# Kernel tuning notes

Hardware: AMD Instinct MI355X
Metric: run time of the kernel (lower is better)

Reference implementation:

```python
import jax, jax.numpy as jnp
import numpy as np

B, LQ, LD = 64, 20, 512
D, NB, WIN = 300, 11, 5
EQ, ED, DESC, KC = 5, 10, 20, 10
VW, VE, VC = 50000, 10000, 5000

# KNRM kernel centers / widths (requires_grad=False buffers in the original)
MU = jnp.array([1.0, 0.9, 0.7, 0.5, 0.3, 0.1, -0.1, -0.3, -0.5, -0.7, -0.9], jnp.float32)
SIGMA = jnp.array([1e-3] + [0.1] * 10, jnp.float32)


def setup_inputs() -> dict:
    key = jax.random.key(0)
    ks = jax.random.split(key, 20)
    f = lambda k, s, sc: jax.random.normal(k, s, jnp.float32) * sc
    return {
        "inputs_qwt": jax.random.randint(ks[0], (B, LQ), 0, VW),
        "inputs_qwm": jnp.ones((B, LQ), jnp.float32),
        "inputs_qei": jax.random.randint(ks[1], (B, EQ), 0, VE),
        "inputs_qet": jax.random.randint(ks[2], (B, EQ * DESC), 0, VW),
        "inputs_qew": jax.random.randint(ks[3], (B, EQ * KC), 0, VC),
        "inputs_qem": jnp.ones((B, EQ), jnp.float32),
        "inputs_dwt": jax.random.randint(ks[4], (B, LD), 0, VW),
        "inputs_dwm": jnp.ones((B, LD), jnp.float32),
        "inputs_dei": jax.random.randint(ks[5], (B, ED), 0, VE),
        "inputs_det": jax.random.randint(ks[6], (B, ED * DESC), 0, VW),
        "inputs_dew": jax.random.randint(ks[7], (B, ED * KC), 0, VC),
        "inputs_dem": jnp.ones((B, ED), jnp.float32),
        "wrd_emb": f(ks[8], (VW, D), 0.1),
        "ent_emb": f(ks[9], (VE, 128), 0.1),
        "car_emb": f(ks[10], (VC, 128), 0.1),
        "bow_W": f(ks[11], (128, D), 0.05), "bow_b": jnp.zeros((128,), jnp.float32),
        "conv_uni_W": f(ks[12], (128, 1, D), 0.05), "conv_uni_b": jnp.zeros((128,), jnp.float32),
        "conv_bi_W": f(ks[13], (128, 2, D), 0.04), "conv_bi_b": jnp.zeros((128,), jnp.float32),
        "conv_tri_W": f(ks[14], (128, 3, D), 0.03), "conv_tri_b": jnp.zeros((128,), jnp.float32),
        "conv_des_W": f(ks[15], (128, WIN, D), 0.02), "conv_des_b": jnp.zeros((128,), jnp.float32),
        "dense_f_W": f(ks[16], (1, 16 * NB), 0.1), "dense_f_b": jnp.zeros((1,), jnp.float32),
    }


def _conv_words(x, w, b):
    # x: [N, L, D]; w: [O, k, D] -> relu conv over the word axis, valid padding -> [N, L-k+1, O]
    k, L = w.shape[1], x.shape[1]
    segs = jnp.stack([x[:, i:L - k + 1 + i] for i in range(k)], axis=2)  # [N, L-k+1, k, D]
    return jax.nn.relu(jnp.einsum('nlkd,okd->nlo', segs, w) + b)


def _l2(x):
    return x / jnp.maximum(jnp.linalg.norm(x, axis=-1, keepdims=True), 1e-10)


def _kernel_pool(q, d, mq, md):
    # q:[B,Lq,128] d:[B,Ld,128] mq:[B,Lq] md:[B,Ld] -> [B, NB]
    sim = jnp.einsum('bqe,bde->bqd', q, d)
    pv = jnp.exp(-0.5 * (sim[..., None] - MU) ** 2 / (SIGMA ** 2)) * md[:, None, :, None]
    lps = jnp.log(jnp.maximum(pv.sum(2), 1e-10)) * 0.01 * mq[:, :, None]
    return lps.sum(1)


def _forward(inputs_qwt, inputs_qwm, inputs_qei, inputs_qet, inputs_qew, inputs_qem,
             inputs_dwt, inputs_dwm, inputs_dei, inputs_det, inputs_dew, inputs_dem,
             wrd_emb, ent_emb, car_emb, bow_W, bow_b,
             conv_uni_W, conv_uni_b, conv_bi_W, conv_bi_b, conv_tri_W, conv_tri_b,
             conv_des_W, conv_des_b, dense_f_W, dense_f_b):
    b = inputs_qwt.shape[0]
    qw = wrd_emb[inputs_qwt]  # [B, LQ, D]
    dw = wrd_emb[inputs_dwt]  # [B, LD, D]

    def ent_branch(ids_e, ids_desc, ids_car, n_ent, w_bow):
        desc = wrd_emb[ids_desc].reshape(b * n_ent, DESC, D)
        e_conv = _conv_words(desc, conv_des_W, conv_des_b).max(1).reshape(b, n_ent, 128)
        t = car_emb[ids_car].reshape(b, n_ent * KC, 128)
        att = jax.nn.softmax((w_bow * t).sum(2).reshape(b, n_ent, KC, 1), axis=2)
        ew = (att * t.reshape(b, n_ent, KC, 128)).sum(2)
        return ent_emb[ids_e] + e_conv + ew

    qw_bow = (jnp.einsum('bld,od->blo', qw, bow_W) + bow_b).sum(1, keepdims=True)  # [B,1,128]
    dw_bow = (jnp.einsum('bld,od->blo', dw, bow_W) + bow_b).sum(1, keepdims=True)
    qs = _l2(ent_branch(inputs_qei, inputs_qet, inputs_qew, EQ, qw_bow))  # [B,5,128]
    ds = _l2(ent_branch(inputs_dei, inputs_det, inputs_dew, ED, dw_bow))  # [B,10,128]

    qu = _l2(_conv_words(qw, conv_uni_W, conv_uni_b))
    qb = _l2(_conv_words(qw, conv_bi_W, conv_bi_b))
    qt = _l2(_conv_words(qw, conv_tri_W, conv_tri_b))
    du = _l2(_conv_words(dw, conv_uni_W, conv_uni_b))
    db = _l2(_conv_words(dw, conv_bi_W, conv_bi_b))
    dt = _l2(_conv_words(dw, conv_tri_W, conv_tri_b))

    mqu, mqb, mqt = inputs_qwm, inputs_qwm[:, :-1], inputs_qwm[:, :-2]
    mdu, mdb, mdt = inputs_dwm, inputs_dwm[:, :-1], inputs_dwm[:, :-2]

    kp = _kernel_pool
    pools = [kp(qu, du, mqu, mdu), kp(qu, dt, mqu, mdt), kp(qu, db, mqu, mdb),
             kp(qb, du, mqb, mdu), kp(qt, du, mqt, mdu), kp(qb, db, mqb, mdb),
             kp(qb, dt, mqb, mdt), kp(qt, db, mqt, mdb), kp(qt, dt, mqt, mdt),
             kp(qs, du, inputs_qem, mdu), kp(qs, db, inputs_qem, mdb), kp(qs, dt, inputs_qem, mdt),
             kp(qu, ds, mqu, inputs_dem), kp(qb, ds, mqb, inputs_dem), kp(qt, ds, mqt, inputs_dem),
             kp(qs, ds, inputs_qem, inputs_dem)]
    feats = jnp.concatenate(pools, axis=1)  # [B, 16*NB]
    return jnp.tanh(feats @ dense_f_W.T + dense_f_b)[:, 0]


def reference(inputs_qwt, inputs_qwm, inputs_qei, inputs_qet, inputs_qew, inputs_qem,
              inputs_dwt, inputs_dwm, inputs_dei, inputs_det, inputs_dew, inputs_dem,
              wrd_emb, ent_emb, car_emb, bow_W, bow_b,
              conv_uni_W, conv_uni_b, conv_bi_W, conv_bi_b, conv_tri_W, conv_tri_b,
              conv_des_W, conv_des_b, dense_f_W, dense_f_b):
    return _forward(inputs_qwt, inputs_qwm, inputs_qei, inputs_qet, inputs_qew, inputs_qem,
                    inputs_dwt, inputs_dwm, inputs_dei, inputs_det, inputs_dew, inputs_dem,
                    wrd_emb, ent_emb, car_emb, bow_W, bow_b,
                    conv_uni_W, conv_uni_b, conv_bi_W, conv_bi_b, conv_tri_W, conv_tri_b,
                    conv_des_W, conv_des_b, dense_f_W, dense_f_b)
```

## Files before the change

### kernel.cpp

```cpp
#include <hip/hip_runtime.h>

typedef unsigned short u16;
typedef unsigned int u32;
typedef __attribute__((ext_vector_type(8))) short bf16x8;
typedef __attribute__((ext_vector_type(4))) float f32x4;

#define DEVI __device__ __forceinline__

namespace {
constexpr int LQ_ = 20, LD_ = 512, D_ = 300;
constexpr int EQ_ = 5, ED_ = 10, KC_ = 10;
constexpr int QROWS = 62, DROWS = 1543;
constexpr int QSTR = 64, DSTR = 1600;
constexpr int XDOC0 = 0;
constexpr int XQ0   = 32768;
constexpr int XQD0  = 34048;
constexpr int XDD0  = 40448;
constexpr int XNR   = 53248;
constexpr float MU_H[11] = {1.0f,0.9f,0.7f,0.5f,0.3f,0.1f,-0.1f,-0.3f,-0.5f,-0.7f,-0.9f};
}

__constant__ int P2QT_C[16] = {0,0,0,1,2,1,1,2,2,3,3,3,0,1,2,3};
__constant__ int P2DT_C[16] = {0,2,1,0,0,1,2,1,2,0,1,2,3,3,3,3};
__constant__ int NP_C[4]   = {2,2,4,4};
__constant__ int PPL_C[16] = {0,1,0,0, 2,3,0,0, 2,3,4,5, 4,5,6,7};
__constant__ int SETL_C[16]= {0,0,0,0, 0,0,0,0, 1,1,0,0, 1,1,0,0};

DEVI u16 f2bf(float f){ union{float f;u32 u;} v; v.f=f; u32 r=(v.u+0x7fffu+((v.u>>16)&1u))>>16; return (u16)r; }
DEVI float bf2f(u16 h){ union{u32 u;float f;} v; v.u=((u32)h)<<16; return v.f; }

__global__ __launch_bounds__(256) void k_prep(const int* __restrict__ dwt, const int* __restrict__ qwt,
                                              const int* __restrict__ qet, const int* __restrict__ det,
                                              const float* __restrict__ emb, u16* __restrict__ xall,
                                              const float* __restrict__ Wu, const float* __restrict__ Wb,
                                              const float* __restrict__ Wt, const float* __restrict__ Wd,
                                              u16* __restrict__ Wp){
  const int bx = blockIdx.x;
  if(bx < 16640){
    long idx = (long)bx*256 + threadIdx.x;
    int row = (int)(idx/80), q = (int)(idx - (long)row*80);
    int tid;
    if(row < XQ0) tid = dwt[row];
    else if(row < XQD0) tid = qwt[row-XQ0];
    else if(row < XDD0) tid = qet[row-XQD0];
    else tid = det[row-XDD0];
    ushort4 o4;
    if(q < 75){
      float4 v = ((const float4*)(emb + (long)tid*D_))[q];
      o4.x=f2bf(v.x); o4.y=f2bf(v.y); o4.z=f2bf(v.z); o4.w=f2bf(v.w);
    } else { o4.x=0;o4.y=0;o4.z=0;o4.w=0; }
    *(ushort4*)(xall + (long)row*320 + q*4) = o4;
  } else {
    const int b2 = bx - 16640;
    const int ts = b2/10, ks = b2 - ts*10;
    const float* W; int kk, tap;
    if(ts==0){W=Wu;kk=1;tap=0;}
    else if(ts<3){W=Wb;kk=2;tap=ts-1;}
    else if(ts<6){W=Wt;kk=3;tap=ts-3;}
    else {W=Wd;kk=5;tap=ts-6;}
    for(int idx=threadIdx.x; idx<4096; idx+=256){
      int n0=idx>>9, lane=(idx>>3)&63, j=idx&7;
      int col=lane&15, kg=lane>>4;
      int d=ks*32+kg*8+j, o=n0*16+col;
      float v = (d<300)? W[((long)o*kk + tap)*300 + d] : 0.f;
      Wp[(((long)(ts*8+n0)*10+ks)*64 + lane)*8 + j] = f2bf(v);
    }
  }
}

__global__ __launch_bounds__(512) void k_main(const u16* __restrict__ xall, const u16* __restrict__ Wp,
    const float* __restrict__ bu, const float* __restrict__ bb, const float* __restrict__ bt,
    u16* __restrict__ dcat, u16* __restrict__ qcat, float* __restrict__ parts)
{
  __shared__ __align__(16) char smem[76576];
  const int bx = blockIdx.x, t = threadIdx.x;
  if(bx < 576){
    const bool isdoc = bx < 512;
    const int seq   = isdoc? (bx>>3) : (bx-512);
    const int l0    = isdoc? (bx&7)*64 : 0;
    const int Ltok  = isdoc? LD_ : LQ_;
    const int rowbase = isdoc? XDOC0 : XQ0;
    u16* outp = isdoc? dcat : qcat;
    const long seqstride = isdoc? (long)DSTR*128 : (long)QSTR*128;
    u16* xs = (u16*)smem;
    float* ot = (float*)(smem + 43296);
    const int nrows = min(66, Ltok - l0);
    const u16* src = xall + ((long)(rowbase + seq*Ltok + l0))*320;
    {
      const bf16x8 z = {0,0,0,0,0,0,0,0};
      for(int idx=t; idx<66*40; idx+=512){
        int r=idx/40, cc=idx-r*40;
        bf16x8 v = *(const bf16x8*)&src[(long)r*320 + cc*8];
        *(bf16x8*)&xs[r*328 + cc*8] = (r<nrows)? v : z;
      }
    }
    __syncthreads();
    const int lane=t&63, wave=t>>6;
    const int col16=lane&15, kg=lane>>4;
    #pragma unroll
    for(int c=0;c<3;c++){
      const int tb = (c==0)?0:((c==1)?1:3);
      const int base = (c==0)?0:((c==1)?Ltok:2*Ltok-1);
      const float* bias = (c==0)?bu:((c==1)?bb:bt);
      f32x4 acc4[4];
      #pragma unroll
      for(int mt=0;mt<4;mt++) acc4[mt]=(f32x4){0.f,0.f,0.f,0.f};
      #pragma unroll
      for(int h=0;h<2;h++){
        bf16x8 wf[15];
        #pragma unroll
        for(int i=0;i<=c;i++)
          #pragma unroll
          for(int k5=0;k5<5;k5++)
            wf[i*5+k5] = *(const bf16x8*)(Wp + (((long)((tb+i)*8 + wave)*10) + h*5 + k5)*512 + lane*8);
        #pragma unroll
        for(int mt=0;mt<4;mt++){
          #pragma unroll
          for(int i=0;i<=c;i++){
            const u16* xrow = &xs[(mt*16 + col16 + i)*328 + h*160];
            #pragma unroll
            for(int k5=0;k5<5;k5++){
              bf16x8 a = *(const bf16x8*)(xrow + k5*32 + kg*8);
              acc4[mt]=__builtin_amdgcn_mfma_f32_16x16x32_bf16(a,wf[i*5+k5],acc4[mt],0,0,0);
            }
          }
        }
      }
      const float bv = bias[wave*16+col16];
      #pragma unroll
      for(int mt=0;mt<4;mt++)
        #pragma unroll
        for(int reg=0;reg<4;reg++)
          ot[(mt*16+kg*4+reg)*130 + wave*16+col16] = fmaxf(acc4[mt][reg]+bv, 0.f);
      __syncthreads();
      {
        const int p = t>>3, j = t&7;
        const int nv = min(64, (Ltok - c) - l0);
        float ss=0.f;
        if(p<nv){
          #pragma unroll
          for(int k=0;k<16;k++){ float v = ot[p*130 + j + 8*k]; ss += v*v; }
        }
        ss += __shfl_xor(ss,1); ss += __shfl_xor(ss,2); ss += __shfl_xor(ss,4);
        if(p<nv){
          float inv = 1.0f/fmaxf(sqrtf(ss),1e-10f);
          u16* ob = outp + (long)seq*seqstride + ((long)(base + l0 + p))*128 + j*16;
          #pragma unroll
          for(int hh=0;hh<2;hh++){
            bf16x8 o8;
            #pragma unroll
            for(int e=0;e<8;e++) o8[e] = (short)f2bf(ot[p*130 + j*16 + hh*8 + e]*inv);
            *(bf16x8*)(ob + hh*8) = o8;
          }
        }
      }
      __syncthreads();
    }
  } else {
    const int idx = bx - 576;
    const int side = idx>>6, b = idx&63;
    const int q = t%80, g = t/80;
    if(g<6){
      float a0=0.f,a1=0.f,a2=0.f,a3=0.f;
      const int L = side? LD_ : LQ_;
      const long base = side? ((long)b*LD_)*320 : ((long)(XQ0 + b*LQ_))*320;
      for(int r=g; r<L; r+=6){
        ushort4 v = *(const ushort4*)(xall + base + (long)r*320 + q*4);
        a0+=bf2f(v.x); a1+=bf2f(v.y); a2+=bf2f(v.z); a3+=bf2f(v.w);
      }
      if(q<76){
        float4 o4={a0,a1,a2,a3};
        *(float4*)(parts + (((long)side*64 + b)*8 + g)*304 + q*4) = o4;
      }
    }
  }
}

__global__ __launch_bounds__(512) void k_desc(const u16* __restrict__ xall,
    const u16* __restrict__ Wp, const float* __restrict__ bd,
    float* __restrict__ qdm, float* __restrict__ ddm)
{
  const int t=threadIdx.x, lane=t&63, wave=t>>6;
  const int col16=lane&15, kg=lane>>4;
  const bool isq = blockIdx.x < 80;
  const int s0 = (isq? blockIdx.x : blockIdx.x-80)*4;
  const int rowbase = isq? XQD0 : XDD0;
  float* dm = isq? qdm : ddm;
  __shared__ u16 xs4[4*20*328];
  {
    for(int idx=t; idx<4*20*40; idx+=512){
      int s=idx/800, rem=idx-s*800, r=rem/40, cc=rem-r*40;
      *(bf16x8*)&xs4[(s*20+r)*328 + cc*8] =
        *(const bf16x8*)&xall[((long)(rowbase + (s0+s)*20 + r))*320 + cc*8];
    }
  }
  __syncthreads();
  f32x4 acc4[4];
  #pragma unroll
  for(int s=0;s<4;s++) acc4[s]=(f32x4){0.f,0.f,0.f,0.f};
  #pragma unroll
  for(int h=0;h<2;h++){
    bf16x8 wf[25];
    #pragma unroll
    for(int tap=0;tap<5;tap++)
      #pragma unroll
      for(int k5=0;k5<5;k5++)
        wf[tap*5+k5] = *(const bf16x8*)(Wp + (((long)((6+tap)*8 + wave)*10) + h*5 + k5)*512 + lane*8);
    #pragma unroll
    for(int s=0;s<4;s++){
      #pragma unroll
      for(int tap=0;tap<5;tap++){
        const u16* xrow = &xs4[(s*20 + col16 + tap)*328 + h*160];
        #pragma unroll
        for(int k5=0;k5<5;k5++){
          bf16x8 a = *(const bf16x8*)(xrow + k5*32 + kg*8);
          acc4[s]=__builtin_amdgcn_mfma_f32_16x16x32_bf16(a,wf[tap*5+k5],acc4[s],0,0,0);
        }
      }
    }
  }
  const float bv = bd[wave*16+col16];
  #pragma unroll
  for(int s=0;s<4;s++){
    float m=-1e30f;
    #pragma unroll
    for(int reg=0;reg<4;reg++) m=fmaxf(m, acc4[s][reg]+bv);
    m=fmaxf(m,__shfl_xor(m,16));
    m=fmaxf(m,__shfl_xor(m,32));
    m=fmaxf(m,0.f);
    if(kg==0) dm[(long)(s0+s)*128 + wave*16+col16]=m;
  }
}

__global__ __launch_bounds__(256) void k_entpost(
    const int* __restrict__ qei, const int* __restrict__ qew,
    const int* __restrict__ dei, const int* __restrict__ dew,
    const float* __restrict__ qdm, const float* __restrict__ ddm,
    const float* __restrict__ parts, const float* __restrict__ bowW, const float* __restrict__ bowb,
    const float* __restrict__ ent, const float* __restrict__ car,
    u16* __restrict__ qcat, u16* __restrict__ dcat)
{
  const int e15 = blockIdx.x, b = blockIdx.y, t = threadIdx.x;
  const bool isq = (e15 < EQ_);
  const int e = isq? e15 : e15-EQ_;
  const float* dmx = isq? (qdm + (long)(b*EQ_+e)*128) : (ddm + (long)(b*ED_+e)*128);
  const int eid = isq? qei[b*EQ_+e] : dei[b*ED_+e];
  const int* carids = isq? (qew + b*EQ_*KC_ + e*KC_) : (dew + b*ED_*KC_ + e*KC_);
  u16* orow = isq? (qcat + ((long)b*QSTR + 57 + e)*128) : (dcat + ((long)b*DSTR + 1533 + e)*128);

  __shared__ float carS[KC_*128];
  __shared__ float sv[304];
  __shared__ float bwS[128];
  __shared__ float sc[KC_], att[KC_];
  __shared__ float red[4];
  const float* p = parts + (((long)(isq?0:1)*64 + b)*8)*304;
  for(int d=t; d<304; d+=256){
    float s=0.f;
    #pragma unroll
    for(int g=0;g<6;g++) s += p[g*304+d];
    sv[d]=s;
  }
  for(int idx=t; idx<KC_*128; idx+=256){
    int j = idx>>7, c = idx&127;
    carS[j*128+c] = car[(long)carids[j]*128 + c];
  }
  __syncthreads();
  {
    const int ch = t>>1, h = t&1;
    float acc=0.f;
    const float* w = bowW + (long)ch*300 + h*150;
    const float* x = sv + h*150;
    for(int d=0; d<150; d++) acc += x[d]*w[d];
    acc += __shfl_xor(acc,1);
    if(h==0) bwS[ch] = acc + (isq? (float)LQ_ : (float)LD_)*bowb[ch];
  }
  __syncthreads();
  {
    const int j = t>>4, l16 = t&15;
    if(j < KC_){
      float s=0.f;
      for(int c=l16;c<128;c+=16) s += bwS[c]*carS[j*128+c];
      s += __shfl_xor(s,1); s += __shfl_xor(s,2); s += __shfl_xor(s,4); s += __shfl_xor(s,8);
      if(l16==0) sc[j]=s;
    }
  }
  __syncthreads();
  if(t==0){
    float m=-1e30f;
    for(int x=0;x<KC_;x++) m = fmaxf(m, sc[x]);
    float ssum=0.f;
    for(int x=0;x<KC_;x++){ float e2=__expf(sc[x]-m); att[x]=e2; ssum+=e2; }
    float rs = 1.0f/ssum;
    for(int x=0;x<KC_;x++) att[x]*=rs;
  }
  __syncthreads();
  float val=0.f;
  if(t<128){
    float ew=0.f;
    for(int x=0;x<KC_;x++) ew += att[x]*carS[x*128+t];
    val = ent[(long)eid*128+t] + dmx[t] + ew;
  }
  float ss = val*val;
  ss += __shfl_xor(ss,1); ss += __shfl_xor(ss,2); ss += __shfl_xor(ss,4);
  ss += __shfl_xor(ss,8); ss += __shfl_xor(ss,16); ss += __shfl_xor(ss,32);
  if((t&63)==0) red[t>>6]=ss;
  __syncthreads();
  if(t<128){
    float nv = 1.0f/fmaxf(sqrtf(red[0]+red[1]),1e-10f);
    orow[t] = f2bf(val*nv);
  }
}

__global__ __launch_bounds__(512) void k_simgauss(const u16* __restrict__ qcat, const u16* __restrict__ dcat,
                                                  const float* __restrict__ dwm, const float* __restrict__ dem,
                                                  float* __restrict__ Spart){
  const int b=blockIdx.x, piece=blockIdx.y;
  const int t=threadIdx.x, lane=t&63, wave=t>>6;
  const int qtile=wave>>1, dpar=wave&1;
  const int col16=lane&15, kg=lane>>4;
  constexpr int NT[4]={8,8,8,1};
  constexpr int TBASE[4]={0,8,16,24};
  constexpr int PEND[4]={512,1023,1533,1543};
  bf16x8 afr[4];
  #pragma unroll
  for(int ks=0;ks<4;ks++)
    afr[ks] = *(const bf16x8*)&qcat[((long)b*QSTR + qtile*16+col16)*128 + ks*32 + kg*8];
  float aP[4][11], aS[4][11];
  #pragma unroll
  for(int r=0;r<4;r++)
    #pragma unroll
    for(int m=0;m<11;m++){ aP[r][m]=0.f; aS[r][m]=0.f; }
  const int t0 = dpar*4;
  const int t1 = (NT[piece] < t0+4)? NT[piece] : t0+4;
  for(int tt=t0; tt<t1; tt++){
    const int tb = TBASE[piece]+tt;
    f32x4 acc[4];
    #pragma unroll
    for(int n0=0;n0<4;n0++) acc[n0]=(f32x4){0.f,0.f,0.f,0.f};
    #pragma unroll
    for(int ks=0;ks<4;ks++){
      #pragma unroll
      for(int n0=0;n0<4;n0++){
        bf16x8 bfr = *(const bf16x8*)&dcat[((long)b*DSTR + tb*64 + n0*16+col16)*128 + ks*32 + kg*8];
        acc[n0]=__builtin_amdgcn_mfma_f32_16x16x32_bf16(afr[ks],bfr,acc[n0],0,0,0);
      }
    }
    #pragma unroll
    for(int n0=0;n0<4;n0++){
      const int col = tb*64 + n0*16 + col16;
      float md;
      if(col<512) md = dwm[b*LD_+col];
      else if(col<1023) md = dwm[b*LD_+col-512];
      else if(col<1533) md = dwm[b*LD_+col-1023];
      else if(col<1543) md = dem[b*ED_+(col-1533)];
      else md = 0.f;
      const bool pr = col < PEND[piece];
      const float mdP = pr? md : 0.f;
      const float mdS = pr? 0.f : md;
      #pragma unroll
      for(int reg=0;reg<4;reg++){
        const float svv = acc[n0][reg];
        {
          float d1 = svv-1.0f;
          float e = __expf(-500000.0f*d1*d1);
          aP[reg][0] += mdP*e; aS[reg][0] += mdS*e;
        }
        #pragma unroll
        for(int m=1;m<11;m++){
          float dm = svv-MU_H[m];
          float e = __expf(-50.0f*dm*dm);
          aP[reg][m] += mdP*e; aS[reg][m] += mdS*e;
        }
      }
    }
  }
  #pragma unroll
  for(int reg=0;reg<4;reg++)
    #pragma unroll
    for(int m=0;m<11;m++){
      float vP=aP[reg][m];
      vP+=__shfl_xor(vP,1); vP+=__shfl_xor(vP,2); vP+=__shfl_xor(vP,4); vP+=__shfl_xor(vP,8);
      aP[reg][m]=vP;
      float vS=aS[reg][m];
      vS+=__shfl_xor(vS,1); vS+=__shfl_xor(vS,2); vS+=__shfl_xor(vS,4); vS+=__shfl_xor(vS,8);
      aS[reg][m]=vS;
    }
  if(col16==0){
    #pragma unroll
    for(int reg=0;reg<4;reg++){
      const int qr = qtile*16 + kg*4 + reg;
      float* o = Spart + (((long)b*64 + qr)*8 + piece*2+dpar)*22;
      #pragma unroll
      for(int m=0;m<11;m++){ o[m]=aP[reg][m]; o[11+m]=aS[reg][m]; }
    }
  }
}

__global__ __launch_bounds__(256) void k_feats(const float* __restrict__ Spart, const float* __restrict__ qwm,
                                               const float* __restrict__ qem, const float* __restrict__ dfW,
                                               const float* __restrict__ dfb, float* __restrict__ out){
  const int b = blockIdx.x, t = threadIdx.x;
  __shared__ float fsh[176];
  __shared__ float red[4];
  if(t<176){
    const int pool = t/11, m = t - pool*11;
    const int qt = P2QT_C[pool], dt = P2DT_C[pool];
    const int qlo = (qt==0)?0:((qt==1)?20:((qt==2)?39:57));
    const int qn  = (qt==0)?20:((qt==1)?19:((qt==2)?18:5));
    float f = 0.f;
    for(int r=0;r<qn;r++){
      const int qr = qlo + r;
      float mq = (qt<3)? qwm[b*LQ_+r] : qem[b*EQ_+r];
      const float* row = Spart + (((long)b*64 + qr)*8)*22 + m;
      float sv = 0.f;
      const int np = NP_C[dt];
      for(int k=0;k<np;k++){
        const int ii = dt*4+k;
        sv += row[PPL_C[ii]*22 + SETL_C[ii]*11];
      }
      f += logf(fmaxf(sv,1e-10f))*0.01f*mq;
    }
    fsh[t] = f;
  }
  __syncthreads();
  float v = (t<176)? fsh[t]*dfW[t] : 0.f;
  v += __shfl_xor(v,1); v += __shfl_xor(v,2); v += __shfl_xor(v,4);
  v += __shfl_xor(v,8); v += __shfl_xor(v,16); v += __shfl_xor(v,32);
  if((t&63)==0) red[t>>6]=v;
  __syncthreads();
  if(t==0) out[b] = tanhf(red[0]+red[1]+red[2]+red[3] + dfb[0]);
}

extern "C" void kernel_launch(void* const* d_in, const int* in_sizes, int n_in,
                              void* d_out, int out_size, void* d_ws, size_t ws_size,
                              hipStream_t stream)
{
  const int*   qwt=(const int*)d_in[0];
  const float* qwm=(const float*)d_in[1];
  const int*   qei=(const int*)d_in[2];
  const int*   qet=(const int*)d_in[3];
  const int*   qew=(const int*)d_in[4];
  const float* qem=(const float*)d_in[5];
  const int*   dwt=(const int*)d_in[6];
  const float* dwm=(const float*)d_in[7];
  const int*   dei=(const int*)d_in[8];
  const int*   det=(const int*)d_in[9];
  const int*   dew=(const int*)d_in[10];
  const float* dem=(const float*)d_in[11];
  const float* emb=(const float*)d_in[12];
  const float* ent=(const float*)d_in[13];
  const float* car=(const float*)d_in[14];
  const float* bowW=(const float*)d_in[15];
  const float* bowb=(const float*)d_in[16];
  const float* Wu=(const float*)d_in[17];
  const float* bu=(const float*)d_in[18];
  const float* Wb=(const float*)d_in[19];
  const float* bb=(const float*)d_in[20];
  const float* Wt=(const float*)d_in[21];
  const float* bt=(const float*)d_in[22];
  const float* Wd=(const float*)d_in[23];
  const float* bd=(const float*)d_in[24];
  const float* dfW=(const float*)d_in[25];
  const float* dfb=(const float*)d_in[26];
  float* out=(float*)d_out;

  char* ws=(char*)d_ws;
  size_t off=0;
  auto A=[&](size_t n){ size_t r=off; off=(off+n+255)&~(size_t)255; return r; };
  u16* Wp     = (u16*)(ws + A((size_t)11*8*10*64*8*2));
  u16* dcat   = (u16*)(ws + A((size_t)64*DSTR*128*2));
  u16* qcat   = (u16*)(ws + A((size_t)64*QSTR*128*2));
  float* qdm  = (float*)(ws + A((size_t)320*128*4));
  float* ddm  = (float*)(ws + A((size_t)640*128*4));
  float* parts= (float*)(ws + A((size_t)2*64*8*304*4));
  float* Spart= (float*)(ws + A((size_t)64*64*8*22*4));
  u16*   xall = (u16*)(ws + A((size_t)XNR*320*2));
  if(off > ws_size) return;

  k_prep<<<16750,256,0,stream>>>(dwt,qwt,qet,det,emb,xall,Wu,Wb,Wt,Wd,Wp);
  k_main<<<704,512,0,stream>>>(xall,Wp,bu,bb,bt,dcat,qcat,parts);
  k_desc<<<240,512,0,stream>>>(xall,Wp,bd,qdm,ddm);
  k_entpost<<<dim3(15,64),256,0,stream>>>(qei,qew,dei,dew,qdm,ddm,parts,bowW,bowb,ent,car,qcat,dcat);
  k_simgauss<<<dim3(64,4),512,0,stream>>>(qcat,dcat,dwm,dem,Spart);
  k_feats<<<64,256,0,stream>>>(Spart,qwm,qem,dfW,dfb,out);
}
```

Measured before the change: 176.4 us.

## Fuse uni/bi/tri conv passes sharing A-fragment loads and register-side normalization

The three word convolutions (uni, bi, tri) now run in one pass: each LDS A-fragment is loaded once and fed to the MFMAs of every conv width that uses that tap, instead of being reloaded for each width. The L2 norm is computed from registers with lane shuffles and a small cross-wave partial-sum buffer, replacing the full fp32 output tile in shared memory and two barriers per conv. This cuts LDS traffic and shared memory size, which may allow more resident blocks. In exchange it keeps three accumulator sets live, raising register pressure, and output stores become scalar 2-byte writes instead of 16-byte vectors.

```diff
diff --git a/kernel.cpp b/kernel.cpp
--- a/kernel.cpp
+++ b/kernel.cpp
@@ -72,7 +72,7 @@
     const float* __restrict__ bu, const float* __restrict__ bb, const float* __restrict__ bt,
     u16* __restrict__ dcat, u16* __restrict__ qcat, float* __restrict__ parts)
 {
-  __shared__ __align__(16) char smem[76576];
+  __shared__ __align__(16) char smem[50208];
   const int bx = blockIdx.x, t = threadIdx.x;
   if(bx < 576){
     const bool isdoc = bx < 512;
@@ -83,7 +83,8 @@
     u16* outp = isdoc? dcat : qcat;
     const long seqstride = isdoc? (long)DSTR*128 : (long)QSTR*128;
     u16* xs = (u16*)smem;
-    float* ot = (float*)(smem + 43296);
+    float* part = (float*)(smem + 43296);
+    float* invA = (float*)(smem + 43296 + 6144);
     const int nrows = min(66, Ltok - l0);
     const u16* src = xall + ((long)(rowbase + seq*Ltok + l0))*320;
     {
@@ -97,64 +98,89 @@
     __syncthreads();
     const int lane=t&63, wave=t>>6;
     const int col16=lane&15, kg=lane>>4;
-    #pragma unroll
-    for(int c=0;c<3;c++){
-      const int tb = (c==0)?0:((c==1)?1:3);
-      const int base = (c==0)?0:((c==1)?Ltok:2*Ltok-1);
-      const float* bias = (c==0)?bu:((c==1)?bb:bt);
-      f32x4 acc4[4];
-      #pragma unroll
-      for(int mt=0;mt<4;mt++) acc4[mt]=(f32x4){0.f,0.f,0.f,0.f};
-      #pragma unroll
-      for(int h=0;h<2;h++){
-        bf16x8 wf[15];
+    f32x4 aU[4], aB[4], aT[4];
+    #pragma unroll
+    for(int mt=0;mt<4;mt++){
+      aU[mt]=(f32x4){0.f,0.f,0.f,0.f};
+      aB[mt]=(f32x4){0.f,0.f,0.f,0.f};
+      aT[mt]=(f32x4){0.f,0.f,0.f,0.f};
+    }
+    #pragma unroll
+    for(int h=0;h<2;h++){
+      #pragma unroll
+      for(int i=0;i<3;i++){
         #pragma unroll
-        for(int i=0;i<=c;i++)
+        for(int k5=0;k5<5;k5++){
+          const long wboff = ((long)h*5 + k5)*512 + lane*8;
+          bf16x8 av[4];
           #pragma unroll
-          for(int k5=0;k5<5;k5++)
-            wf[i*5+k5] = *(const bf16x8*)(Wp + (((long)((tb+i)*8 + wave)*10) + h*5 + k5)*512 + lane*8);
-        #pragma unroll
-        for(int mt=0;mt<4;mt++){
-          #pragma unroll
-          for(int i=0;i<=c;i++){
-            const u16* xrow = &xs[(mt*16 + col16 + i)*328 + h*160];
+          for(int mt=0;mt<4;mt++)
+            av[mt] = *(const bf16x8*)&xs[(mt*16+col16+i)*328 + h*160 + k5*32 + kg*8];
+          {
+            bf16x8 wT = *(const bf16x8*)(Wp + ((long)((3+i)*8+wave)*10)*512 + wboff);
             #pragma unroll
-            for(int k5=0;k5<5;k5++){
-              bf16x8 a = *(const bf16x8*)(xrow + k5*32 + kg*8);
-              acc4[mt]=__builtin_amdgcn_mfma_f32_16x16x32_bf16(a,wf[i*5+k5],acc4[mt],0,0,0);
-            }
+            for(int mt=0;mt<4;mt++)
+              aT[mt]=__builtin_amdgcn_mfma_f32_16x16x32_bf16(av[mt],wT,aT[mt],0,0,0);
+          }
+          if(i<2){
+            bf16x8 wB = *(const bf16x8*)(Wp + ((long)((1+i)*8+wave)*10)*512 + wboff);
+            #pragma unroll
+            for(int mt=0;mt<4;mt++)
+              aB[mt]=__builtin_amdgcn_mfma_f32_16x16x32_bf16(av[mt],wB,aB[mt],0,0,0);
+          }
+          if(i==0){
+            bf16x8 wU = *(const bf16x8*)(Wp + ((long)(wave)*10)*512 + wboff);
+            #pragma unroll
+            for(int mt=0;mt<4;mt++)
+              aU[mt]=__builtin_amdgcn_mfma_f32_16x16x32_bf16(av[mt],wU,aU[mt],0,0,0);
           }
         }
       }
-      const float bv = bias[wave*16+col16];
-      #pragma unroll
-      for(int mt=0;mt<4;mt++)
-        #pragma unroll
-        for(int reg=0;reg<4;reg++)
-          ot[(mt*16+kg*4+reg)*130 + wave*16+col16] = fmaxf(acc4[mt][reg]+bv, 0.f);
-      __syncthreads();
-      {
-        const int p = t>>3, j = t&7;
-        const int nv = min(64, (Ltok - c) - l0);
-        float ss=0.f;
-        if(p<nv){
-          #pragma unroll
-          for(int k=0;k<16;k++){ float v = ot[p*130 + j + 8*k]; ss += v*v; }
+    }
+    const float bvU = bu[wave*16+col16];
+    const float bvB = bb[wave*16+col16];
+    const float bvT = bt[wave*16+col16];
+    #pragma unroll
+    for(int mt=0;mt<4;mt++){
+      #pragma unroll
+      for(int reg=0;reg<4;reg++){
+        float vU = fmaxf(aU[mt][reg]+bvU, 0.f); aU[mt][reg]=vU;
+        float vB = fmaxf(aB[mt][reg]+bvB, 0.f); aB[mt][reg]=vB;
+        float vT = fmaxf(aT[mt][reg]+bvT, 0.f); aT[mt][reg]=vT;
+        float sU = vU*vU, sB = vB*vB, sT = vT*vT;
+        sU += __shfl_xor(sU,1); sU += __shfl_xor(sU,2); sU += __shfl_xor(sU,4); sU += __shfl_xor(sU,8);
+        sB += __shfl_xor(sB,1); sB += __shfl_xor(sB,2); sB += __shfl_xor(sB,4); sB += __shfl_xor(sB,8);
+        sT += __shfl_xor(sT,1); sT += __shfl_xor(sT,2); sT += __shfl_xor(sT,4); sT += __shfl_xor(sT,8);
+        if(col16==0){
+          const int row = mt*16 + kg*4 + reg;
+          part[wave*192 + 0*64 + row] = sU;
+          part[wave*192 + 1*64 + row] = sB;
+          part[wave*192 + 2*64 + row] = sT;
         }
-        ss += __shfl_xor(ss,1); ss += __shfl_xor(ss,2); ss += __shfl_xor(ss,4);
-        if(p<nv){
-          float inv = 1.0f/fmaxf(sqrtf(ss),1e-10f);
-          u16* ob = outp + (long)seq*seqstride + ((long)(base + l0 + p))*128 + j*16;
-          #pragma unroll
-          for(int hh=0;hh<2;hh++){
-            bf16x8 o8;
-            #pragma unroll
-            for(int e=0;e<8;e++) o8[e] = (short)f2bf(ot[p*130 + j*16 + hh*8 + e]*inv);
-            *(bf16x8*)(ob + hh*8) = o8;
-          }
-        }
-      }
-      __syncthreads();
+      }
+    }
+    __syncthreads();
+    if(t<192){
+      float s=0.f;
+      #pragma unroll
+      for(int w=0;w<8;w++) s += part[w*192+t];
+      invA[t] = 1.0f/fmaxf(sqrtf(s),1e-10f);
+    }
+    __syncthreads();
+    const int nvU = min(64, Ltok   - l0);
+    const int nvB = min(64, Ltok-1 - l0);
+    const int nvT = min(64, Ltok-2 - l0);
+    u16* ob = outp + (long)seq*seqstride;
+    #pragma unroll
+    for(int mt=0;mt<4;mt++){
+      #pragma unroll
+      for(int reg=0;reg<4;reg++){
+        const int p = mt*16 + kg*4 + reg;
+        const long ch = wave*16 + col16;
+        if(p < nvU) ob[((long)(l0+p))*128 + ch]            = f2bf(aU[mt][reg]*invA[0*64+p]);
+        if(p < nvB) ob[((long)(Ltok+l0+p))*128 + ch]       = f2bf(aB[mt][reg]*invA[1*64+p]);
+        if(p < nvT) ob[((long)(2*Ltok-1+l0+p))*128 + ch]   = f2bf(aT[mt][reg]*invA[2*64+p]);
+      }
     }
   } else {
     const int idx = bx - 576;
@@ -210,10 +236,10 @@
     for(int s=0;s<4;s++){
       #pragma unroll
       for(int tap=0;tap<5;tap++){
-        const u16* xrow = &xs4[(s*20 + col16 + tap)*328 + h*160];
+        const u16* xrow = &xs4[(s*20 + col16 + tap)*328 + h*160 + kg*8];
         #pragma unroll
         for(int k5=0;k5<5;k5++){
-          bf16x8 a = *(const bf16x8*)(xrow + k5*32 + kg*8);
+          bf16x8 a = *(const bf16x8*)(xrow + k5*32);
           acc4[s]=__builtin_amdgcn_mfma_f32_16x16x32_bf16(a,wf[tap*5+k5],acc4[s],0,0,0);
         }
       }
```

Result: slower. 181.5 us (+2.9%).

## Merge description conv into main conv kernel and halve per-block tiles

Applied to the files above, without the earlier changes.

Folds the separate description-conv kernel into k_main as an extra block range, removing one launch and letting its blocks run alongside the word-conv blocks. Document word tiles shrink from 64 to 32 positions and description blocks from 4 to 2 sequences, which cuts shared memory per block and roughly doubles the grid for better occupancy and load balance. The cost is more halo reloads of input rows and weight fragments per unit of work. The ot stride also changes to 132 and the normalize/write phase is remapped to 16 threads per row.

```diff
diff --git a/kernel.cpp b/kernel.cpp
--- a/kernel.cpp
+++ b/kernel.cpp
@@ -70,41 +70,42 @@
 
 __global__ __launch_bounds__(512) void k_main(const u16* __restrict__ xall, const u16* __restrict__ Wp,
     const float* __restrict__ bu, const float* __restrict__ bb, const float* __restrict__ bt,
-    u16* __restrict__ dcat, u16* __restrict__ qcat, float* __restrict__ parts)
+    const float* __restrict__ bd,
+    u16* __restrict__ dcat, u16* __restrict__ qcat,
+    float* __restrict__ qdm, float* __restrict__ ddm, float* __restrict__ parts)
 {
-  __shared__ __align__(16) char smem[76576];
+  __shared__ __align__(16) char smem[39424];
   const int bx = blockIdx.x, t = threadIdx.x;
-  if(bx < 576){
-    const bool isdoc = bx < 512;
-    const int seq   = isdoc? (bx>>3) : (bx-512);
-    const int l0    = isdoc? (bx&7)*64 : 0;
+  const int lane=t&63, wave=t>>6, col16=lane&15, kg=lane>>4;
+  if(bx < 1088){
+    const bool isdoc = bx < 1024;
+    const int seq   = isdoc? (bx>>4) : (bx-1024);
+    const int l0    = isdoc? (bx&15)*32 : 0;
     const int Ltok  = isdoc? LD_ : LQ_;
     const int rowbase = isdoc? XDOC0 : XQ0;
     u16* outp = isdoc? dcat : qcat;
     const long seqstride = isdoc? (long)DSTR*128 : (long)QSTR*128;
     u16* xs = (u16*)smem;
-    float* ot = (float*)(smem + 43296);
-    const int nrows = min(66, Ltok - l0);
+    float* ot = (float*)(smem + 22304);
+    const int nrows = min(34, Ltok - l0);
     const u16* src = xall + ((long)(rowbase + seq*Ltok + l0))*320;
     {
       const bf16x8 z = {0,0,0,0,0,0,0,0};
-      for(int idx=t; idx<66*40; idx+=512){
+      for(int idx=t; idx<34*40; idx+=512){
         int r=idx/40, cc=idx-r*40;
         bf16x8 v = *(const bf16x8*)&src[(long)r*320 + cc*8];
         *(bf16x8*)&xs[r*328 + cc*8] = (r<nrows)? v : z;
       }
     }
     __syncthreads();
-    const int lane=t&63, wave=t>>6;
-    const int col16=lane&15, kg=lane>>4;
     #pragma unroll
     for(int c=0;c<3;c++){
       const int tb = (c==0)?0:((c==1)?1:3);
       const int base = (c==0)?0:((c==1)?Ltok:2*Ltok-1);
       const float* bias = (c==0)?bu:((c==1)?bb:bt);
-      f32x4 acc4[4];
-      #pragma unroll
-      for(int mt=0;mt<4;mt++) acc4[mt]=(f32x4){0.f,0.f,0.f,0.f};
+      f32x4 acc4[2];
+      #pragma unroll
+      for(int mt=0;mt<2;mt++) acc4[mt]=(f32x4){0.f,0.f,0.f,0.f};
       #pragma unroll
       for(int h=0;h<2;h++){
         bf16x8 wf[15];
@@ -114,13 +115,13 @@
           for(int k5=0;k5<5;k5++)
             wf[i*5+k5] = *(const bf16x8*)(Wp + (((long)((tb+i)*8 + wave)*10) + h*5 + k5)*512 + lane*8);
         #pragma unroll
-        for(int mt=0;mt<4;mt++){
+        for(int mt=0;mt<2;mt++){
           #pragma unroll
           for(int i=0;i<=c;i++){
-            const u16* xrow = &xs[(mt*16 + col16 + i)*328 + h*160];
+            const u16* xrow = &xs[(mt*16 + col16 + i)*328 + h*160 + kg*8];
             #pragma unroll
             for(int k5=0;k5<5;k5++){
-              bf16x8 a = *(const bf16x8*)(xrow + k5*32 + kg*8);
+              bf16x8 a = *(const bf16x8*)(xrow + k5*32);
               acc4[mt]=__builtin_amdgcn_mfma_f32_16x16x32_bf16(a,wf[i*5+k5],acc4[mt],0,0,0);
             }
           }
@@ -128,36 +129,83 @@
       }
       const float bv = bias[wave*16+col16];
       #pragma unroll
-      for(int mt=0;mt<4;mt++)
+      for(int mt=0;mt<2;mt++)
         #pragma unroll
         for(int reg=0;reg<4;reg++)
-          ot[(mt*16+kg*4+reg)*130 + wave*16+col16] = fmaxf(acc4[mt][reg]+bv, 0.f);
+          ot[(mt*16+kg*4+reg)*132 + wave*16+col16] = fmaxf(acc4[mt][reg]+bv, 0.f);
       __syncthreads();
       {
-        const int p = t>>3, j = t&7;
-        const int nv = min(64, (Ltok - c) - l0);
+        const int p = t>>4, j = t&15;
+        const int nv = min(32, (Ltok - c) - l0);
         float ss=0.f;
         if(p<nv){
           #pragma unroll
-          for(int k=0;k<16;k++){ float v = ot[p*130 + j + 8*k]; ss += v*v; }
-        }
-        ss += __shfl_xor(ss,1); ss += __shfl_xor(ss,2); ss += __shfl_xor(ss,4);
+          for(int k=0;k<8;k++){ float v = ot[p*132 + j + 16*k]; ss += v*v; }
+        }
+        ss += __shfl_xor(ss,1); ss += __shfl_xor(ss,2); ss += __shfl_xor(ss,4); ss += __shfl_xor(ss,8);
         if(p<nv){
           float inv = 1.0f/fmaxf(sqrtf(ss),1e-10f);
-          u16* ob = outp + (long)seq*seqstride + ((long)(base + l0 + p))*128 + j*16;
+          u16* ob = outp + (long)seq*seqstride + ((long)(base + l0 + p))*128 + j*8;
+          bf16x8 o8;
           #pragma unroll
-          for(int hh=0;hh<2;hh++){
-            bf16x8 o8;
-            #pragma unroll
-            for(int e=0;e<8;e++) o8[e] = (short)f2bf(ot[p*130 + j*16 + hh*8 + e]*inv);
-            *(bf16x8*)(ob + hh*8) = o8;
+          for(int e=0;e<8;e++) o8[e] = (short)f2bf(ot[p*132 + j*8 + e]*inv);
+          *(bf16x8*)ob = o8;
+        }
+      }
+      __syncthreads();
+    }
+  } else if(bx < 1568){
+    const int d = bx - 1088;
+    const bool isq = d < 160;
+    const int s0 = (isq? d : d-160)*2;
+    const int rowbase = isq? XQD0 : XDD0;
+    float* dm = isq? qdm : ddm;
+    u16* xs2 = (u16*)smem;
+    {
+      for(int idx=t; idx<2*20*40; idx+=512){
+        int s=idx/800, rem=idx-s*800, r=rem/40, cc=rem-r*40;
+        *(bf16x8*)&xs2[(s*20+r)*328 + cc*8] =
+          *(const bf16x8*)&xall[((long)(rowbase + (s0+s)*20 + r))*320 + cc*8];
+      }
+    }
+    __syncthreads();
+    f32x4 acc4[2];
+    #pragma unroll
+    for(int s=0;s<2;s++) acc4[s]=(f32x4){0.f,0.f,0.f,0.f};
+    #pragma unroll
+    for(int h=0;h<2;h++){
+      bf16x8 wf[25];
+      #pragma unroll
+      for(int tap=0;tap<5;tap++)
+        #pragma unroll
+        for(int k5=0;k5<5;k5++)
+          wf[tap*5+k5] = *(const bf16x8*)(Wp + (((long)((6+tap)*8 + wave)*10) + h*5 + k5)*512 + lane*8);
+      #pragma unroll
+      for(int s=0;s<2;s++){
+        #pragma unroll
+        for(int tap=0;tap<5;tap++){
+          const u16* xrow = &xs2[(s*20 + col16 + tap)*328 + h*160 + kg*8];
+          #pragma unroll
+          for(int k5=0;k5<5;k5++){
+            bf16x8 a = *(const bf16x8*)(xrow + k5*32);
+            acc4[s]=__builtin_amdgcn_mfma_f32_16x16x32_bf16(a,wf[tap*5+k5],acc4[s],0,0,0);
           }
         }
       }
-      __syncthreads();
+    }
+    const float bv = bd[wave*16+col16];
+    #pragma unroll
+    for(int s=0;s<2;s++){
+      float m=-1e30f;
+      #pragma unroll
+      for(int reg=0;reg<4;reg++) m=fmaxf(m, acc4[s][reg]+bv);
+      m=fmaxf(m,__shfl_xor(m,16));
+      m=fmaxf(m,__shfl_xor(m,32));
+      m=fmaxf(m,0.f);
+      if(kg==0) dm[(long)(s0+s)*128 + wave*16+col16]=m;
     }
   } else {
-    const int idx = bx - 576;
+    const int idx = bx - 1568;
     const int side = idx>>6, b = idx&63;
     const int q = t%80, g = t/80;
     if(g<6){
@@ -173,62 +221,6 @@
         *(float4*)(parts + (((long)side*64 + b)*8 + g)*304 + q*4) = o4;
       }
     }
-  }
-}
-
-__global__ __launch_bounds__(512) void k_desc(const u16* __restrict__ xall,
-    const u16* __restrict__ Wp, const float* __restrict__ bd,
-    float* __restrict__ qdm, float* __restrict__ ddm)
-{
-  const int t=threadIdx.x, lane=t&63, wave=t>>6;
-  const int col16=lane&15, kg=lane>>4;
-  const bool isq = blockIdx.x < 80;
-  const int s0 = (isq? blockIdx.x : blockIdx.x-80)*4;
-  const int rowbase = isq? XQD0 : XDD0;
-  float* dm = isq? qdm : ddm;
-  __shared__ u16 xs4[4*20*328];
-  {
-    for(int idx=t; idx<4*20*40; idx+=512){
-      int s=idx/800, rem=idx-s*800, r=rem/40, cc=rem-r*40;
-      *(bf16x8*)&xs4[(s*20+r)*328 + cc*8] =
-        *(const bf16x8*)&xall[((long)(rowbase + (s0+s)*20 + r))*320 + cc*8];
-    }
-  }
-  __syncthreads();
-  f32x4 acc4[4];
-  #pragma unroll
-  for(int s=0;s<4;s++) acc4[s]=(f32x4){0.f,0.f,0.f,0.f};
-  #pragma unroll
-  for(int h=0;h<2;h++){
-    bf16x8 wf[25];
-    #pragma unroll
-    for(int tap=0;tap<5;tap++)
-      #pragma unroll
-      for(int k5=0;k5<5;k5++)
-        wf[tap*5+k5] = *(const bf16x8*)(Wp + (((long)((6+tap)*8 + wave)*10) + h*5 + k5)*512 + lane*8);
-    #pragma unroll
-    for(int s=0;s<4;s++){
-      #pragma unroll
-      for(int tap=0;tap<5;tap++){
-        const u16* xrow = &xs4[(s*20 + col16 + tap)*328 + h*160];
-        #pragma unroll
-        for(int k5=0;k5<5;k5++){
-          bf16x8 a = *(const bf16x8*)(xrow + k5*32 + kg*8);
-          acc4[s]=__builtin_amdgcn_mfma_f32_16x16x32_bf16(a,wf[tap*5+k5],acc4[s],0,0,0);
-        }
-      }
-    }
-  }
-  const float bv = bd[wave*16+col16];
-  #pragma unroll
-  for(int s=0;s<4;s++){
-    float m=-1e30f;
-    #pragma unroll
-    for(int reg=0;reg<4;reg++) m=fmaxf(m, acc4[s][reg]+bv);
-    m=fmaxf(m,__shfl_xor(m,16));
-    m=fmaxf(m,__shfl_xor(m,32));
-    m=fmaxf(m,0.f);
-    if(kg==0) dm[(long)(s0+s)*128 + wave*16+col16]=m;
   }
 }
 
@@ -478,8 +470,7 @@
   if(off > ws_size) return;
 
   k_prep<<<16750,256,0,stream>>>(dwt,qwt,qet,det,emb,xall,Wu,Wb,Wt,Wd,Wp);
-  k_main<<<704,512,0,stream>>>(xall,Wp,bu,bb,bt,dcat,qcat,parts);
-  k_desc<<<240,512,0,stream>>>(xall,Wp,bd,qdm,ddm);
+  k_main<<<1696,512,0,stream>>>(xall,Wp,bu,bb,bt,bd,dcat,qcat,qdm,ddm,parts);
   k_entpost<<<dim3(15,64),256,0,stream>>>(qei,qew,dei,dew,qdm,ddm,parts,bowW,bowb,ent,car,qcat,dcat);
   k_simgauss<<<dim3(64,4),512,0,stream>>>(qcat,dcat,dwm,dem,Spart);
   k_feats<<<64,256,0,stream>>>(Spart,qwm,qem,dfW,dfb,out);
```

New measurement: 176.5 us. About the same (+0.1%).
